# Kernel tuning notes

Measured on AMD Instinct MI355X. Metric: run time of the kernel, lower is better.

The kernel has to match this reference:

```python
import jax, jax.numpy as jnp
import numpy as np
import math

B, N0, DEG = 32, 1584, 4
E = B * N0 * DEG
FIN, HID, EDIM, ROUTE, HEADS = 32, 64, 8, 16, 4
NEG = 0.2  # leaky_relu negative slope (alpha)
K1 = math.ceil(0.8 * N0)   # 1268 nodes/graph after pool1
K2 = math.ceil(0.8 * K1)   # 1015 after pool2
K3 = math.ceil(0.8 * K2)   # 812 after pool3


def _gatv2(x, src, dst, emask, edge_attr, Wl, bl, Wr, br, We, att, bo, num_nodes):
    # PyG GATv2Conv, concat=False (mean over heads), edge_dim, eval mode (no dropout)
    xl = (x @ Wl + bl).reshape(-1, HEADS, HID)            # source transform  [N,H,C]
    xr = (x @ Wr + br).reshape(-1, HEADS, HID)            # target transform  [N,H,C]
    ee = (edge_attr @ We).reshape(-1, HEADS, HID)         # edge transform    [E,H,C]
    m = jax.nn.leaky_relu(xl[src] + xr[dst] + ee, NEG)    # [E,H,C]
    logits = jnp.einsum('ehc,hc->eh', m, att)             # [E,H]
    logits = jnp.where(emask[:, None], logits, -jnp.inf)
    mx = jax.ops.segment_max(logits, dst, num_segments=num_nodes)
    mx = jnp.where(jnp.isfinite(mx), mx, 0.0)             # nodes w/o in-edges
    ex = jnp.where(emask[:, None], jnp.exp(logits - mx[dst]), 0.0)
    den = jax.ops.segment_sum(ex, dst, num_segments=num_nodes)
    alpha = ex / jnp.maximum(den[dst], 1e-16)             # segment softmax over dst
    out = jax.ops.segment_sum(alpha[:, :, None] * xl[src], dst, num_segments=num_nodes)
    return out.mean(axis=1) + bo                          # concat=False -> head mean


def _topk(x, src, dst, emask, w, n_per, k):
    # PyG TopKPooling(ratio=0.8): score = tanh(x.w/||w||); keep top-k per graph,
    # scale kept features by score; keep edges whose endpoints both survive.
    s = jnp.tanh((x @ w) / jnp.linalg.norm(w))            # [B*n_per]
    _, idx = jax.lax.top_k(s.reshape(B, n_per), k)        # [B,k]
    perm = (idx + jnp.arange(B)[:, None] * n_per).reshape(-1)
    x_new = x[perm] * s[perm][:, None]
    new_id = jnp.full((B * n_per,), -1, jnp.int32).at[perm].set(
        jnp.arange(B * k, dtype=jnp.int32))
    nsrc, ndst = new_id[src], new_id[dst]
    m = emask & (nsrc >= 0) & (ndst >= 0)
    return x_new, jnp.where(m, nsrc, 0), jnp.where(m, ndst, 0), m


def _readout(x, k):
    # global mean pool || global max pool (nodes are grouped per graph, k each)
    xb = x.reshape(B, k, HID)
    return jnp.concatenate([xb.mean(1), xb.max(1)], axis=1)


def _forward(x, edge_attr, edge_index,
             g1_Wl, g1_bl, g1_Wr, g1_br, g1_We, g1_att, g1_b,
             g2_Wl, g2_bl, g2_Wr, g2_br, g2_We, g2_att, g2_b,
             g3_Wl, g3_bl, g3_Wr, g3_br, g3_We, g3_att, g3_b,
             p1_w, p2_w, p3_w,
             fc1_W, fc1_b, fc2_W, fc2_b, fc3_W, fc3_b):
    src, dst = edge_index[0], edge_index[1]
    emask = jnp.ones((E,), bool)
    h = jax.nn.relu(_gatv2(x, src, dst, emask, edge_attr,
                           g1_Wl, g1_bl, g1_Wr, g1_br, g1_We, g1_att, g1_b, B * N0))
    h, src, dst, emask = _topk(h, src, dst, emask, p1_w, N0, K1)
    x1 = _readout(h, K1)
    h = jax.nn.relu(_gatv2(h, src, dst, emask, edge_attr,
                           g2_Wl, g2_bl, g2_Wr, g2_br, g2_We, g2_att, g2_b, B * K1))
    h, src, dst, emask = _topk(h, src, dst, emask, p2_w, K1, K2)
    x2 = _readout(h, K2)
    h = jax.nn.relu(_gatv2(h, src, dst, emask, edge_attr,
                           g3_Wl, g3_bl, g3_Wr, g3_br, g3_We, g3_att, g3_b, B * K2))
    h, src, dst, emask = _topk(h, src, dst, emask, p3_w, K2, K3)
    x3 = _readout(h, K3)
    r = x1 + x2 + x3                                      # [B, 2*HID]
    h = jax.nn.relu(r @ fc1_W + fc1_b)
    h = jax.nn.relu(h @ fc2_W + fc2_b)                    # dropout results unused in source
    return jax.nn.softmax(h @ fc3_W + fc3_b, axis=1)      # [B, ROUTE]


def setup_inputs() -> dict:
    key = jax.random.key(0)
    ks = iter(jax.random.split(key, 64))
    def nrm(shape, scale):
        return jax.random.normal(next(ks), shape, jnp.float32) * scale
    x = nrm((B * N0, FIN), 1.0)
    srcl = jax.random.randint(next(ks), (B, N0 * DEG), 0, N0)
    dstl = jax.random.randint(next(ks), (B, N0 * DEG), 0, N0)
    off = (jnp.arange(B) * N0)[:, None]
    edge_index = jnp.stack([(srcl + off).reshape(-1),
                            (dstl + off).reshape(-1)]).astype(jnp.int32)
    edge_attr = nrm((E, EDIM), 1.0)
    batch = jnp.repeat(jnp.arange(B, dtype=jnp.int32), N0)
    inp = {"x": x, "edge_attr": edge_attr, "edge_index": edge_index, "batch": batch}
    for li, fin in ((1, FIN), (2, HID), (3, HID)):
        g = 1.0 / np.sqrt(fin)
        inp[f"g{li}_Wl"] = nrm((fin, HEADS * HID), g)
        inp[f"g{li}_bl"] = nrm((HEADS * HID,), 0.02)
        inp[f"g{li}_Wr"] = nrm((fin, HEADS * HID), g)
        inp[f"g{li}_br"] = nrm((HEADS * HID,), 0.02)
        inp[f"g{li}_We"] = nrm((EDIM, HEADS * HID), 1.0 / np.sqrt(EDIM))
        inp[f"g{li}_att"] = nrm((HEADS, HID), 1.0 / np.sqrt(HID))
        inp[f"g{li}_b"] = nrm((HID,), 0.02)
    for li in (1, 2, 3):
        inp[f"p{li}_w"] = nrm((HID,), 1.0 / np.sqrt(HID))
    for fin, fout, nm in ((2 * HID, HID, "fc1"), (HID, HID, "fc2"), (HID, ROUTE, "fc3")):
        inp[f"{nm}_W"] = nrm((fin, fout), 1.0 / np.sqrt(fin))
        inp[f"{nm}_b"] = nrm((fout,), 0.02)
    return inp


def reference(x, edge_attr, edge_index, batch,
              g1_Wl, g1_bl, g1_Wr, g1_br, g1_We, g1_att, g1_b,
              g2_Wl, g2_bl, g2_Wr, g2_br, g2_We, g2_att, g2_b,
              g3_Wl, g3_bl, g3_Wr, g3_br, g3_We, g3_att, g3_b,
              p1_w, p2_w, p3_w,
              fc1_W, fc1_b, fc2_W, fc2_b, fc3_W, fc3_b):
    # batch is implicit: nodes are laid out grouped per graph with static sizes
    del batch
    return _forward(x, edge_attr, edge_index,
                    g1_Wl, g1_bl, g1_Wr, g1_br, g1_We, g1_att, g1_b,
                    g2_Wl, g2_bl, g2_Wr, g2_br, g2_We, g2_att, g2_b,
                    g3_Wl, g3_bl, g3_Wr, g3_br, g3_We, g3_att, g3_b,
                    p1_w, p2_w, p3_w,
                    fc1_W, fc1_b, fc2_W, fc2_b, fc3_W, fc3_b)
```

## Files before the change

### kernel.cpp

```cpp
#include <hip/hip_runtime.h>

typedef unsigned short u16;
typedef unsigned int u32;
typedef unsigned long long u64;

#define E_TOT 202752
#define NMAX  50688
#define HEADS 4
#define B_    32
#define MAXDEG 32

#define CDIV(a,b) (((a)+(b)-1)/(b))

__device__ __forceinline__ u32 ford(float f) {
  u32 u = __float_as_uint(f);
  return (u & 0x80000000u) ? ~u : (u | 0x80000000u);
}
__device__ __forceinline__ float ford_inv(u32 u) {
  u32 b = (u & 0x80000000u) ? (u ^ 0x80000000u) : ~u;
  return __uint_as_float(b);
}

__global__ void k_edge_init_csr(const int* __restrict__ ei, int* __restrict__ src,
                                int* __restrict__ dst, int* __restrict__ em,
                                int* __restrict__ cnt, int* __restrict__ csr) {
  int e = blockIdx.x * blockDim.x + threadIdx.x;
  if (e >= E_TOT) return;
  int s = ei[e], d = ei[E_TOT + e];
  src[e] = s;
  dst[e] = d;
  em[e] = 1;
  int pos = atomicAdd(&cnt[d], 1);
  if (pos < MAXDEG) csr[d * MAXDEG + pos] = e;
}

template <int FIN>
__global__ void k_transform_t(const float* __restrict__ hin,
                              const float* __restrict__ Wl, const float* __restrict__ bl,
                              const float* __restrict__ Wr, const float* __restrict__ br,
                              float* __restrict__ xl, float* __restrict__ xr) {
  __shared__ float xs[FIN][20];
  int n0 = blockIdx.x * 16, j = threadIdx.x;
  for (int t = j; t < 16 * FIN; t += 256) {
    int nd = t >> (FIN == 32 ? 5 : 6), f = t & (FIN - 1);
    xs[f][nd] = hin[(size_t)(n0 + nd) * FIN + f];
  }
  __syncthreads();
  float al[16], ar[16];
  float blv = bl[j], brv = br[j];
#pragma unroll
  for (int t = 0; t < 16; ++t) { al[t] = blv; ar[t] = brv; }
  for (int i = 0; i < FIN; ++i) {
    float wl = Wl[i * 256 + j], wr = Wr[i * 256 + j];
    float4 x0 = *(const float4*)&xs[i][0];
    float4 x1 = *(const float4*)&xs[i][4];
    float4 x2 = *(const float4*)&xs[i][8];
    float4 x3 = *(const float4*)&xs[i][12];
    al[0]  += x0.x * wl; ar[0]  += x0.x * wr;
    al[1]  += x0.y * wl; ar[1]  += x0.y * wr;
    al[2]  += x0.z * wl; ar[2]  += x0.z * wr;
    al[3]  += x0.w * wl; ar[3]  += x0.w * wr;
    al[4]  += x1.x * wl; ar[4]  += x1.x * wr;
    al[5]  += x1.y * wl; ar[5]  += x1.y * wr;
    al[6]  += x1.z * wl; ar[6]  += x1.z * wr;
    al[7]  += x1.w * wl; ar[7]  += x1.w * wr;
    al[8]  += x2.x * wl; ar[8]  += x2.x * wr;
    al[9]  += x2.y * wl; ar[9]  += x2.y * wr;
    al[10] += x2.z * wl; ar[10] += x2.z * wr;
    al[11] += x2.w * wl; ar[11] += x2.w * wr;
    al[12] += x3.x * wl; ar[12] += x3.x * wr;
    al[13] += x3.y * wl; ar[13] += x3.y * wr;
    al[14] += x3.z * wl; ar[14] += x3.z * wr;
    al[15] += x3.w * wl; ar[15] += x3.w * wr;
  }
#pragma unroll
  for (int t = 0; t < 16; ++t) {
    xl[(size_t)(n0 + t) * 256 + j] = al[t];
    xr[(size_t)(n0 + t) * 256 + j] = ar[t];
  }
}

__global__ void k_gat_fused(const int* __restrict__ srcv, const int* __restrict__ cnt,
                            const int* __restrict__ csr, const float* __restrict__ ea,
                            const float* __restrict__ We, const float* __restrict__ att,
                            const float* __restrict__ xl, const float* __restrict__ xr,
                            const float* __restrict__ bias, const float* __restrict__ pwv,
                            float* __restrict__ out, float* __restrict__ sc, int N) {
  int n = blockIdx.x * 4 + (threadIdx.x >> 6);
  int lane = threadIdx.x & 63;
  int cg = lane & 15;
  int cb = (lane >> 4) * 64 + cg * 4;
  if (n >= N) return;
  int deg = min(cnt[n], MAXDEG);
  int e_l = 0, s_l = 0;
  if (lane < deg) { e_l = csr[n * MAXDEG + lane]; s_l = srcv[e_l]; }
  float4 xd4 = *(const float4*)(xr + (size_t)n * 256 + cb);
  float4 at4 = *(const float4*)(att + cb);
  float4 w0 = *(const float4*)(We + 0 * 256 + cb);
  float4 w1 = *(const float4*)(We + 1 * 256 + cb);
  float4 w2 = *(const float4*)(We + 2 * 256 + cb);
  float4 w3 = *(const float4*)(We + 3 * 256 + cb);
  float4 w4_ = *(const float4*)(We + 4 * 256 + cb);
  float4 w5 = *(const float4*)(We + 5 * 256 + cb);
  float4 w6 = *(const float4*)(We + 6 * 256 + cb);
  float4 w7 = *(const float4*)(We + 7 * 256 + cb);
  float4 pw4 = *(const float4*)(pwv + cg * 4);
  float wn = pw4.x * pw4.x + pw4.y * pw4.y + pw4.z * pw4.z + pw4.w * pw4.w;
  wn += __shfl_xor(wn, 1, 64); wn += __shfl_xor(wn, 2, 64);
  wn += __shfl_xor(wn, 4, 64); wn += __shfl_xor(wn, 8, 64);
  float isq = 1.f / sqrtf(wn);
  float m = -INFINITY, l = 0.f;
  float ox = 0.f, oy = 0.f, oz = 0.f, ow = 0.f;
  for (int i0 = 0; i0 < deg; i0 += 4) {
    int c0 = deg - i0; if (c0 > 4) c0 = 4;
    float4 xs[4], a0[4], a1[4];
#pragma unroll
    for (int j = 0; j < 4; ++j) {
      int idx = (j < c0) ? (i0 + j) : i0;
      int e = __shfl(e_l, idx, 64);
      int s = __shfl(s_l, idx, 64);
      xs[j] = *(const float4*)(xl + (size_t)s * 256 + cb);
      a0[j] = *(const float4*)(ea + (size_t)e * 8);
      a1[j] = *(const float4*)(ea + (size_t)e * 8 + 4);
    }
#pragma unroll
    for (int j = 0; j < 4; ++j) {
      if (j < c0) {
        float e0 = a0[j].x * w0.x + a0[j].y * w1.x + a0[j].z * w2.x + a0[j].w * w3.x
                 + a1[j].x * w4_.x + a1[j].y * w5.x + a1[j].z * w6.x + a1[j].w * w7.x;
        float e1 = a0[j].x * w0.y + a0[j].y * w1.y + a0[j].z * w2.y + a0[j].w * w3.y
                 + a1[j].x * w4_.y + a1[j].y * w5.y + a1[j].z * w6.y + a1[j].w * w7.y;
        float e2 = a0[j].x * w0.z + a0[j].y * w1.z + a0[j].z * w2.z + a0[j].w * w3.z
                 + a1[j].x * w4_.z + a1[j].y * w5.z + a1[j].z * w6.z + a1[j].w * w7.z;
        float e3 = a0[j].x * w0.w + a0[j].y * w1.w + a0[j].z * w2.w + a0[j].w * w3.w
                 + a1[j].x * w4_.w + a1[j].y * w5.w + a1[j].z * w6.w + a1[j].w * w7.w;
        float m0 = xs[j].x + xd4.x + e0; m0 = (m0 >= 0.f) ? m0 : 0.2f * m0;
        float m1 = xs[j].y + xd4.y + e1; m1 = (m1 >= 0.f) ? m1 : 0.2f * m1;
        float m2 = xs[j].z + xd4.z + e2; m2 = (m2 >= 0.f) ? m2 : 0.2f * m2;
        float m3 = xs[j].w + xd4.w + e3; m3 = (m3 >= 0.f) ? m3 : 0.2f * m3;
        float v = at4.x * m0 + at4.y * m1 + at4.z * m2 + at4.w * m3;
        v += __shfl_xor(v, 1, 64);
        v += __shfl_xor(v, 2, 64);
        v += __shfl_xor(v, 4, 64);
        v += __shfl_xor(v, 8, 64);
        float nm = fmaxf(m, v);
        float scale = __expf(m - nm);
        float p = __expf(v - nm);
        ox = ox * scale + p * xs[j].x;
        oy = oy * scale + p * xs[j].y;
        oz = oz * scale + p * xs[j].z;
        ow = ow * scale + p * xs[j].w;
        l = l * scale + p;
        m = nm;
      }
    }
  }
  float inv = 0.25f / fmaxf(l, 1e-16f);
  float r0 = ox * inv, r1 = oy * inv, r2 = oz * inv, r3 = ow * inv;
  r0 += __shfl_xor(r0, 16, 64); r0 += __shfl_xor(r0, 32, 64);
  r1 += __shfl_xor(r1, 16, 64); r1 += __shfl_xor(r1, 32, 64);
  r2 += __shfl_xor(r2, 16, 64); r2 += __shfl_xor(r2, 32, 64);
  r3 += __shfl_xor(r3, 16, 64); r3 += __shfl_xor(r3, 32, 64);
  float4 bi4 = *(const float4*)(bias + cg * 4);
  r0 = fmaxf(r0 + bi4.x, 0.f); r1 = fmaxf(r1 + bi4.y, 0.f);
  r2 = fmaxf(r2 + bi4.z, 0.f); r3 = fmaxf(r3 + bi4.w, 0.f);
  if (lane < 16) *(float4*)(out + (size_t)n * 64 + cg * 4) = float4{r0, r1, r2, r3};
  float dot = r0 * pw4.x + r1 * pw4.y + r2 * pw4.z + r3 * pw4.w;
  dot += __shfl_xor(dot, 1, 64);
  dot += __shfl_xor(dot, 2, 64);
  dot += __shfl_xor(dot, 4, 64);
  dot += __shfl_xor(dot, 8, 64);
  if (lane == 0) sc[n] = tanhf(dot * isq);
}

__global__ __launch_bounds__(1024) void k_topk(const float* __restrict__ s, int n_per,
                                               int k, int npad,
                                               int* __restrict__ perm, int* __restrict__ new_id) {
  __shared__ u64 kv[2048];
  int b = blockIdx.x, tid = threadIdx.x;
  int base = b * n_per;
  for (int i = tid; i < n_per; i += 1024) new_id[base + i] = -1;
  for (int i = tid; i < npad; i += 1024) {
    u32 sk = (i < n_per) ? ford(s[base + i]) : 0u;
    kv[i] = ((u64)sk << 32) | (u32)(0xFFFFFFFFu - (u32)i);
  }
  __syncthreads();
  for (int kk = 2; kk <= npad; kk <<= 1) {
    for (int j = kk >> 1; j > 0; j >>= 1) {
      for (int i = tid; i < npad; i += 1024) {
        int ixj = i ^ j;
        if (ixj > i) {
          u64 a = kv[i], c = kv[ixj];
          bool after = a < c;
          bool doswap = ((i & kk) == 0) ? after : !after;
          if (doswap) { kv[i] = c; kv[ixj] = a; }
        }
      }
      __syncthreads();
    }
  }
  for (int r = tid; r < k; r += 1024) {
    int old = (int)(0xFFFFFFFFu - (u32)(kv[r] & 0xFFFFFFFFu));
    perm[b * k + r] = base + old;
    new_id[base + old] = b * k + r;
  }
}

__global__ void k_gather_ro(const float* __restrict__ hin, const float* __restrict__ s,
                            const int* __restrict__ perm, float* __restrict__ hout,
                            int k, float* __restrict__ rsum, u32* __restrict__ rmaxI) {
  __shared__ float ps[256], pm[256];
  int b = blockIdx.x, t = threadIdx.x;
  int i = blockIdx.y * 4 + (t >> 6);
  int c = t & 63;
  bool valid = i < k;
  float v = 0.f;
  if (valid) {
    int g = perm[b * k + i];
    v = hin[(size_t)g * 64 + c] * s[g];
    hout[((size_t)b * k + i) * 64 + c] = v;
  }
  ps[t] = valid ? v : 0.f;
  pm[t] = valid ? v : -INFINITY;
  __syncthreads();
  if (t < 64) {
    float s4 = ps[t] + ps[t + 64] + ps[t + 128] + ps[t + 192];
    float m4 = fmaxf(fmaxf(pm[t], pm[t + 64]), fmaxf(pm[t + 128], pm[t + 192]));
    atomicAdd(&rsum[b * 64 + t], s4);
    atomicMax(&rmaxI[b * 64 + t], ford(m4));
  }
}

__global__ void k_remap_csr(int* __restrict__ src, int* __restrict__ dst,
                            int* __restrict__ em, const int* __restrict__ new_id,
                            int* __restrict__ cnt, int* __restrict__ csr) {
  int e = blockIdx.x * blockDim.x + threadIdx.x;
  if (e >= E_TOT) return;
  int ns = new_id[src[e]], nd = new_id[dst[e]];
  int m = em[e] && ns >= 0 && nd >= 0;
  src[e] = m ? ns : 0;
  dst[e] = m ? nd : 0;
  em[e] = m;
  if (m) {
    int pos = atomicAdd(&cnt[nd], 1);
    if (pos < MAXDEG) csr[nd * MAXDEG + pos] = e;
  }
}

__global__ void k_readout_fin(const float* __restrict__ rsum, const u32* __restrict__ rmaxI,
                              int k, float* __restrict__ r) {
  int b = blockIdx.x, c = threadIdx.x;
  if (c < 64) r[b * 128 + c] += rsum[b * 64 + c] / (float)k;
  else        r[b * 128 + c] += ford_inv(rmaxI[b * 64 + (c - 64)]);
}

__global__ void k_mlp(const float* __restrict__ r,
                      const float* __restrict__ W1, const float* __restrict__ b1,
                      const float* __restrict__ W2, const float* __restrict__ b2,
                      const float* __restrict__ W3, const float* __restrict__ b3,
                      float* __restrict__ out) {
  __shared__ float v0[128], v1[64], v2[64], lgts[16];
  int b = blockIdx.x, t = threadIdx.x;
  v0[t] = r[b * 128 + t];
  v0[64 + t] = r[b * 128 + 64 + t];
  __syncthreads();
  float a = b1[t];
  for (int i = 0; i < 128; ++i) a += v0[i] * W1[i * 64 + t];
  v1[t] = fmaxf(a, 0.f);
  __syncthreads();
  a = b2[t];
  for (int i = 0; i < 64; ++i) a += v1[i] * W2[i * 64 + t];
  v2[t] = fmaxf(a, 0.f);
  __syncthreads();
  if (t < 16) {
    a = b3[t];
    for (int i = 0; i < 64; ++i) a += v2[i] * W3[i * 16 + t];
    lgts[t] = a;
  }
  __syncthreads();
  if (t == 0) {
    float m = lgts[0];
    for (int j = 1; j < 16; ++j) m = fmaxf(m, lgts[j]);
    float ex[16], sum = 0.f;
    for (int j = 0; j < 16; ++j) { ex[j] = expf(lgts[j] - m); sum += ex[j]; }
    for (int j = 0; j < 16; ++j) out[b * 16 + j] = ex[j] / sum;
  }
}

extern "C" void kernel_launch(void* const* d_in, const int* in_sizes, int n_in,
                              void* d_out, int out_size, void* d_ws, size_t ws_size,
                              hipStream_t stream) {
  (void)in_sizes; (void)n_in; (void)out_size; (void)ws_size;
  const float* x  = (const float*)d_in[0];
  const float* ea = (const float*)d_in[1];
  const int*   ei = (const int*)d_in[2];

  const float *gWl[3], *gbl[3], *gWr[3], *gbr[3], *gWe[3], *gatt[3], *gb[3], *pw[3];
  for (int l = 0; l < 3; ++l) {
    int p0 = 4 + 7 * l;
    gWl[l]  = (const float*)d_in[p0 + 0];
    gbl[l]  = (const float*)d_in[p0 + 1];
    gWr[l]  = (const float*)d_in[p0 + 2];
    gbr[l]  = (const float*)d_in[p0 + 3];
    gWe[l]  = (const float*)d_in[p0 + 4];
    gatt[l] = (const float*)d_in[p0 + 5];
    gb[l]   = (const float*)d_in[p0 + 6];
    pw[l]   = (const float*)d_in[25 + l];
  }
  const float* fc1W = (const float*)d_in[28];
  const float* fc1b = (const float*)d_in[29];
  const float* fc2W = (const float*)d_in[30];
  const float* fc2b = (const float*)d_in[31];
  const float* fc3W = (const float*)d_in[32];
  const float* fc3b = (const float*)d_in[33];

  char* w = (char*)d_ws;
  size_t off = 0;
  auto alloc = [&](size_t bytes) -> void* {
    void* p = w + off;
    off += (bytes + 255) & ~(size_t)255;
    return p;
  };
  float* hbuf = (float*)alloc((size_t)B_ * 1268 * 64 * 4);
  float* xl   = (float*)alloc((size_t)NMAX * 256 * 4);
  float* xr   = (float*)alloc((size_t)NMAX * 256 * 4);
  float* nacc = (float*)alloc((size_t)NMAX * 64 * 4);
  int*   cnt  = (int*)alloc((size_t)NMAX * 4);
  char*  rblk = (char*)alloc(3 * 32 * 128 * 4);
  int*   csr  = (int*)alloc((size_t)NMAX * MAXDEG * 4);
  float* sbuf = (float*)alloc((size_t)NMAX * 4);
  float* rbuf = (float*)alloc(32 * 128 * 4);
  int* src    = (int*)alloc((size_t)E_TOT * 4);
  int* dst    = (int*)alloc((size_t)E_TOT * 4);
  int* em     = (int*)alloc((size_t)E_TOT * 4);
  int* new_id = (int*)alloc((size_t)NMAX * 4);
  int* perm   = (int*)alloc((size_t)32 * 1268 * 4);

  hipMemsetAsync(cnt, 0, (size_t)NMAX * 4, stream);
  hipMemsetAsync(rblk, 0, 3 * 32 * 128 * 4, stream);
  hipMemsetAsync(rbuf, 0, 32 * 128 * 4, stream);
  k_edge_init_csr<<<CDIV(E_TOT, 256), 256, 0, stream>>>(ei, src, dst, em, cnt, csr);

  const int Ns[3]    = {50688, 40576, 32480};
  const int npers[3] = {1584, 1268, 1015};
  const int ks[3]    = {1268, 1015, 812};
  const int npads[3] = {2048, 2048, 1024};

  for (int l = 0; l < 3; ++l) {
    int N = Ns[l];
    const float* hin = (l == 0) ? x : hbuf;
    float* rsum = (float*)(rblk + l * 32 * 128 * 4);
    u32* rmaxI  = (u32*)(rblk + l * 32 * 128 * 4 + 32 * 64 * 4);
    if (l == 0)
      k_transform_t<32><<<N / 16, 256, 0, stream>>>(hin, gWl[l], gbl[l], gWr[l], gbr[l], xl, xr);
    else
      k_transform_t<64><<<N / 16, 256, 0, stream>>>(hin, gWl[l], gbl[l], gWr[l], gbr[l], xl, xr);
    k_gat_fused<<<N / 4, 256, 0, stream>>>(src, cnt, csr, ea, gWe[l], gatt[l],
                                           xl, xr, gb[l], pw[l], nacc, sbuf, N);
    k_topk<<<32, 1024, 0, stream>>>(sbuf, npers[l], ks[l], npads[l], perm, new_id);
    k_gather_ro<<<dim3(32, CDIV(ks[l], 4)), 256, 0, stream>>>(nacc, sbuf, perm, hbuf,
                                                              ks[l], rsum, rmaxI);
    if (l < 2) {
      hipMemsetAsync(cnt, 0, (size_t)NMAX * 4, stream);
      k_remap_csr<<<CDIV(E_TOT, 256), 256, 0, stream>>>(src, dst, em, new_id, cnt, csr);
    }
    k_readout_fin<<<32, 128, 0, stream>>>(rsum, rmaxI, ks[l], rbuf);
  }
  k_mlp<<<32, 64, 0, stream>>>(rbuf, fc1W, fc1b, fc2W, fc2b, fc3W, fc3b, (float*)d_out);
}
```

Baseline: 550.2 us.

## Make GAT kernel persistent over node ranges and fold readout finalize into MLP

The GAT kernel now launches a fixed 2048-block grid where each wave processes a contiguous range of nodes. This amortizes the per-wave loads of edge weights, attention vector, bias and pooling weight. The per-layer readout finalize kernel and its accumulation buffer are removed, and the MLP kernel reads the three layers' sum/max blocks directly. The trade-off is fewer independent waves for latency hiding on the gather-heavy loop.

```diff
diff --git a/kernel.cpp b/kernel.cpp
--- a/kernel.cpp
+++ b/kernel.cpp
@@ -85,16 +85,14 @@
                             const float* __restrict__ We, const float* __restrict__ att,
                             const float* __restrict__ xl, const float* __restrict__ xr,
                             const float* __restrict__ bias, const float* __restrict__ pwv,
-                            float* __restrict__ out, float* __restrict__ sc, int N) {
-  int n = blockIdx.x * 4 + (threadIdx.x >> 6);
+                            float* __restrict__ out, float* __restrict__ sc,
+                            int N, int npw) {
+  int wid = blockIdx.x * 4 + (threadIdx.x >> 6);
   int lane = threadIdx.x & 63;
   int cg = lane & 15;
   int cb = (lane >> 4) * 64 + cg * 4;
-  if (n >= N) return;
-  int deg = min(cnt[n], MAXDEG);
-  int e_l = 0, s_l = 0;
-  if (lane < deg) { e_l = csr[n * MAXDEG + lane]; s_l = srcv[e_l]; }
-  float4 xd4 = *(const float4*)(xr + (size_t)n * 256 + cb);
+  int n0 = wid * npw, n1 = min(N, n0 + npw);
+  if (n0 >= N) return;
   float4 at4 = *(const float4*)(att + cb);
   float4 w0 = *(const float4*)(We + 0 * 256 + cb);
   float4 w1 = *(const float4*)(We + 1 * 256 + cb);
@@ -104,73 +102,80 @@
   float4 w5 = *(const float4*)(We + 5 * 256 + cb);
   float4 w6 = *(const float4*)(We + 6 * 256 + cb);
   float4 w7 = *(const float4*)(We + 7 * 256 + cb);
+  float4 bi4 = *(const float4*)(bias + cg * 4);
   float4 pw4 = *(const float4*)(pwv + cg * 4);
   float wn = pw4.x * pw4.x + pw4.y * pw4.y + pw4.z * pw4.z + pw4.w * pw4.w;
   wn += __shfl_xor(wn, 1, 64); wn += __shfl_xor(wn, 2, 64);
   wn += __shfl_xor(wn, 4, 64); wn += __shfl_xor(wn, 8, 64);
   float isq = 1.f / sqrtf(wn);
-  float m = -INFINITY, l = 0.f;
-  float ox = 0.f, oy = 0.f, oz = 0.f, ow = 0.f;
-  for (int i0 = 0; i0 < deg; i0 += 4) {
-    int c0 = deg - i0; if (c0 > 4) c0 = 4;
-    float4 xs[4], a0[4], a1[4];
+
+  for (int n = n0; n < n1; ++n) {
+    int deg = min(cnt[n], MAXDEG);
+    int e_l = 0, s_l = 0;
+    if (lane < deg) { e_l = csr[n * MAXDEG + lane]; s_l = srcv[e_l]; }
+    float4 xd4 = *(const float4*)(xr + (size_t)n * 256 + cb);
+    float m = -INFINITY, l = 0.f;
+    float ox = 0.f, oy = 0.f, oz = 0.f, ow = 0.f;
+    for (int i0 = 0; i0 < deg; i0 += 4) {
+      int c0 = deg - i0; if (c0 > 4) c0 = 4;
+      float4 xs[4], a0[4], a1[4];
 #pragma unroll
-    for (int j = 0; j < 4; ++j) {
-      int idx = (j < c0) ? (i0 + j) : i0;
-      int e = __shfl(e_l, idx, 64);
-      int s = __shfl(s_l, idx, 64);
-      xs[j] = *(const float4*)(xl + (size_t)s * 256 + cb);
-      a0[j] = *(const float4*)(ea + (size_t)e * 8);
-      a1[j] = *(const float4*)(ea + (size_t)e * 8 + 4);
-    }
+      for (int j = 0; j < 4; ++j) {
+        int idx = (j < c0) ? (i0 + j) : i0;
+        int e = __shfl(e_l, idx, 64);
+        int s = __shfl(s_l, idx, 64);
+        xs[j] = *(const float4*)(xl + (size_t)s * 256 + cb);
+        a0[j] = *(const float4*)(ea + (size_t)e * 8);
+        a1[j] = *(const float4*)(ea + (size_t)e * 8 + 4);
+      }
 #pragma unroll
-    for (int j = 0; j < 4; ++j) {
-      if (j < c0) {
-        float e0 = a0[j].x * w0.x + a0[j].y * w1.x + a0[j].z * w2.x + a0[j].w * w3.x
-                 + a1[j].x * w4_.x + a1[j].y * w5.x + a1[j].z * w6.x + a1[j].w * w7.x;
-        float e1 = a0[j].x * w0.y + a0[j].y * w1.y + a0[j].z * w2.y + a0[j].w * w3.y
-                 + a1[j].x * w4_.y + a1[j].y * w5.y + a1[j].z * w6.y + a1[j].w * w7.y;
-        float e2 = a0[j].x * w0.z + a0[j].y * w1.z + a0[j].z * w2.z + a0[j].w * w3.z
-                 + a1[j].x * w4_.z + a1[j].y * w5.z + a1[j].z * w6.z + a1[j].w * w7.z;
-        float e3 = a0[j].x * w0.w + a0[j].y * w1.w + a0[j].z * w2.w + a0[j].w * w3.w
-                 + a1[j].x * w4_.w + a1[j].y * w5.w + a1[j].z * w6.w + a1[j].w * w7.w;
-        float m0 = xs[j].x + xd4.x + e0; m0 = (m0 >= 0.f) ? m0 : 0.2f * m0;
-        float m1 = xs[j].y + xd4.y + e1; m1 = (m1 >= 0.f) ? m1 : 0.2f * m1;
-        float m2 = xs[j].z + xd4.z + e2; m2 = (m2 >= 0.f) ? m2 : 0.2f * m2;
-        float m3 = xs[j].w + xd4.w + e3; m3 = (m3 >= 0.f) ? m3 : 0.2f * m3;
-        float v = at4.x * m0 + at4.y * m1 + at4.z * m2 + at4.w * m3;
-        v += __shfl_xor(v, 1, 64);
-        v += __shfl_xor(v, 2, 64);
-        v += __shfl_xor(v, 4, 64);
-        v += __shfl_xor(v, 8, 64);
-        float nm = fmaxf(m, v);
-        float scale = __expf(m - nm);
-        float p = __expf(v - nm);
-        ox = ox * scale + p * xs[j].x;
-        oy = oy * scale + p * xs[j].y;
-        oz = oz * scale + p * xs[j].z;
-        ow = ow * scale + p * xs[j].w;
-        l = l * scale + p;
-        m = nm;
+      for (int j = 0; j < 4; ++j) {
+        if (j < c0) {
+          float e0 = a0[j].x * w0.x + a0[j].y * w1.x + a0[j].z * w2.x + a0[j].w * w3.x
+                   + a1[j].x * w4_.x + a1[j].y * w5.x + a1[j].z * w6.x + a1[j].w * w7.x;
+          float e1 = a0[j].x * w0.y + a0[j].y * w1.y + a0[j].z * w2.y + a0[j].w * w3.y
+                   + a1[j].x * w4_.y + a1[j].y * w5.y + a1[j].z * w6.y + a1[j].w * w7.y;
+          float e2 = a0[j].x * w0.z + a0[j].y * w1.z + a0[j].z * w2.z + a0[j].w * w3.z
+                   + a1[j].x * w4_.z + a1[j].y * w5.z + a1[j].z * w6.z + a1[j].w * w7.z;
+          float e3 = a0[j].x * w0.w + a0[j].y * w1.w + a0[j].z * w2.w + a0[j].w * w3.w
+                   + a1[j].x * w4_.w + a1[j].y * w5.w + a1[j].z * w6.w + a1[j].w * w7.w;
+          float m0 = xs[j].x + xd4.x + e0; m0 = (m0 >= 0.f) ? m0 : 0.2f * m0;
+          float m1 = xs[j].y + xd4.y + e1; m1 = (m1 >= 0.f) ? m1 : 0.2f * m1;
+          float m2 = xs[j].z + xd4.z + e2; m2 = (m2 >= 0.f) ? m2 : 0.2f * m2;
+          float m3 = xs[j].w + xd4.w + e3; m3 = (m3 >= 0.f) ? m3 : 0.2f * m3;
+          float v = at4.x * m0 + at4.y * m1 + at4.z * m2 + at4.w * m3;
+          v += __shfl_xor(v, 1, 64);
+          v += __shfl_xor(v, 2, 64);
+          v += __shfl_xor(v, 4, 64);
+          v += __shfl_xor(v, 8, 64);
+          float nm = fmaxf(m, v);
+          float scale = __expf(m - nm);
+          float p = __expf(v - nm);
+          ox = ox * scale + p * xs[j].x;
+          oy = oy * scale + p * xs[j].y;
+          oz = oz * scale + p * xs[j].z;
+          ow = ow * scale + p * xs[j].w;
+          l = l * scale + p;
+          m = nm;
+        }
       }
     }
-  }
-  float inv = 0.25f / fmaxf(l, 1e-16f);
-  float r0 = ox * inv, r1 = oy * inv, r2 = oz * inv, r3 = ow * inv;
-  r0 += __shfl_xor(r0, 16, 64); r0 += __shfl_xor(r0, 32, 64);
-  r1 += __shfl_xor(r1, 16, 64); r1 += __shfl_xor(r1, 32, 64);
-  r2 += __shfl_xor(r2, 16, 64); r2 += __shfl_xor(r2, 32, 64);
-  r3 += __shfl_xor(r3, 16, 64); r3 += __shfl_xor(r3, 32, 64);
-  float4 bi4 = *(const float4*)(bias + cg * 4);
-  r0 = fmaxf(r0 + bi4.x, 0.f); r1 = fmaxf(r1 + bi4.y, 0.f);
-  r2 = fmaxf(r2 + bi4.z, 0.f); r3 = fmaxf(r3 + bi4.w, 0.f);
-  if (lane < 16) *(float4*)(out + (size_t)n * 64 + cg * 4) = float4{r0, r1, r2, r3};
-  float dot = r0 * pw4.x + r1 * pw4.y + r2 * pw4.z + r3 * pw4.w;
-  dot += __shfl_xor(dot, 1, 64);
-  dot += __shfl_xor(dot, 2, 64);
-  dot += __shfl_xor(dot, 4, 64);
-  dot += __shfl_xor(dot, 8, 64);
-  if (lane == 0) sc[n] = tanhf(dot * isq);
+    float inv = 0.25f / fmaxf(l, 1e-16f);
+    float r0 = ox * inv, r1 = oy * inv, r2 = oz * inv, r3 = ow * inv;
+    r0 += __shfl_xor(r0, 16, 64); r0 += __shfl_xor(r0, 32, 64);
+    r1 += __shfl_xor(r1, 16, 64); r1 += __shfl_xor(r1, 32, 64);
+    r2 += __shfl_xor(r2, 16, 64); r2 += __shfl_xor(r2, 32, 64);
+    r3 += __shfl_xor(r3, 16, 64); r3 += __shfl_xor(r3, 32, 64);
+    float rr0 = fmaxf(r0 + bi4.x, 0.f), rr1 = fmaxf(r1 + bi4.y, 0.f);
+    float rr2 = fmaxf(r2 + bi4.z, 0.f), rr3 = fmaxf(r3 + bi4.w, 0.f);
+    if (lane < 16) *(float4*)(out + (size_t)n * 64 + cg * 4) = float4{rr0, rr1, rr2, rr3};
+    float dot = rr0 * pw4.x + rr1 * pw4.y + rr2 * pw4.z + rr3 * pw4.w;
+    dot += __shfl_xor(dot, 1, 64);
+    dot += __shfl_xor(dot, 2, 64);
+    dot += __shfl_xor(dot, 4, 64);
+    dot += __shfl_xor(dot, 8, 64);
+    if (lane == 0) sc[n] = tanhf(dot * isq);
+  }
 }
 
 __global__ __launch_bounds__(1024) void k_topk(const float* __restrict__ s, int n_per,
@@ -247,22 +252,21 @@
   }
 }
 
-__global__ void k_readout_fin(const float* __restrict__ rsum, const u32* __restrict__ rmaxI,
-                              int k, float* __restrict__ r) {
-  int b = blockIdx.x, c = threadIdx.x;
-  if (c < 64) r[b * 128 + c] += rsum[b * 64 + c] / (float)k;
-  else        r[b * 128 + c] += ford_inv(rmaxI[b * 64 + (c - 64)]);
-}
-
-__global__ void k_mlp(const float* __restrict__ r,
+__global__ void k_mlp(const char* __restrict__ rblk,
                       const float* __restrict__ W1, const float* __restrict__ b1,
                       const float* __restrict__ W2, const float* __restrict__ b2,
                       const float* __restrict__ W3, const float* __restrict__ b3,
                       float* __restrict__ out) {
   __shared__ float v0[128], v1[64], v2[64], lgts[16];
   int b = blockIdx.x, t = threadIdx.x;
-  v0[t] = r[b * 128 + t];
-  v0[64 + t] = r[b * 128 + 64 + t];
+  const float* rs0 = (const float*)rblk;
+  const u32*   rm0 = (const u32*)(rblk + 32 * 64 * 4);
+  const float* rs1 = (const float*)(rblk + 32 * 128 * 4);
+  const u32*   rm1 = (const u32*)(rblk + 32 * 128 * 4 + 32 * 64 * 4);
+  const float* rs2 = (const float*)(rblk + 2 * 32 * 128 * 4);
+  const u32*   rm2 = (const u32*)(rblk + 2 * 32 * 128 * 4 + 32 * 64 * 4);
+  v0[t] = rs0[b * 64 + t] / 1268.f + rs1[b * 64 + t] / 1015.f + rs2[b * 64 + t] / 812.f;
+  v0[64 + t] = ford_inv(rm0[b * 64 + t]) + ford_inv(rm1[b * 64 + t]) + ford_inv(rm2[b * 64 + t]);
   __syncthreads();
   float a = b1[t];
   for (int i = 0; i < 128; ++i) a += v0[i] * W1[i * 64 + t];
@@ -329,7 +333,6 @@
   char*  rblk = (char*)alloc(3 * 32 * 128 * 4);
   int*   csr  = (int*)alloc((size_t)NMAX * MAXDEG * 4);
   float* sbuf = (float*)alloc((size_t)NMAX * 4);
-  float* rbuf = (float*)alloc(32 * 128 * 4);
   int* src    = (int*)alloc((size_t)E_TOT * 4);
   int* dst    = (int*)alloc((size_t)E_TOT * 4);
   int* em     = (int*)alloc((size_t)E_TOT * 4);
@@ -338,13 +341,13 @@
 
   hipMemsetAsync(cnt, 0, (size_t)NMAX * 4, stream);
   hipMemsetAsync(rblk, 0, 3 * 32 * 128 * 4, stream);
-  hipMemsetAsync(rbuf, 0, 32 * 128 * 4, stream);
   k_edge_init_csr<<<CDIV(E_TOT, 256), 256, 0, stream>>>(ei, src, dst, em, cnt, csr);
 
   const int Ns[3]    = {50688, 40576, 32480};
   const int npers[3] = {1584, 1268, 1015};
   const int ks[3]    = {1268, 1015, 812};
   const int npads[3] = {2048, 2048, 1024};
+  const int GAT_BLOCKS = 2048;
 
   for (int l = 0; l < 3; ++l) {
     int N = Ns[l];
@@ -355,8 +358,9 @@
       k_transform_t<32><<<N / 16, 256, 0, stream>>>(hin, gWl[l], gbl[l], gWr[l], gbr[l], xl, xr);
     else
       k_transform_t<64><<<N / 16, 256, 0, stream>>>(hin, gWl[l], gbl[l], gWr[l], gbr[l], xl, xr);
-    k_gat_fused<<<N / 4, 256, 0, stream>>>(src, cnt, csr, ea, gWe[l], gatt[l],
-                                           xl, xr, gb[l], pw[l], nacc, sbuf, N);
+    int npw = CDIV(N, GAT_BLOCKS * 4);
+    k_gat_fused<<<GAT_BLOCKS, 256, 0, stream>>>(src, cnt, csr, ea, gWe[l], gatt[l],
+                                                xl, xr, gb[l], pw[l], nacc, sbuf, N, npw);
     k_topk<<<32, 1024, 0, stream>>>(sbuf, npers[l], ks[l], npads[l], perm, new_id);
     k_gather_ro<<<dim3(32, CDIV(ks[l], 4)), 256, 0, stream>>>(nacc, sbuf, perm, hbuf,
                                                               ks[l], rsum, rmaxI);
@@ -364,7 +368,6 @@
       hipMemsetAsync(cnt, 0, (size_t)NMAX * 4, stream);
       k_remap_csr<<<CDIV(E_TOT, 256), 256, 0, stream>>>(src, dst, em, new_id, cnt, csr);
     }
-    k_readout_fin<<<32, 128, 0, stream>>>(rsum, rmaxI, ks[l], rbuf);
-  }
-  k_mlp<<<32, 64, 0, stream>>>(rbuf, fc1W, fc1b, fc2W, fc2b, fc3W, fc3b, (float*)d_out);
-}
+  }
+  k_mlp<<<32, 64, 0, stream>>>(rblk, fc1W, fc1b, fc2W, fc2b, fc3W, fc3b, (float*)d_out);
+}
```

Result: faster. 535.3 us (-2.7%).
